# Optimization experiments

Hardware: AMD Instinct MI355X
Metric: run time of the kernel (lower is better)

Reference implementation:

```python
import jax, jax.numpy as jnp
import numpy as np

D_MODEL = 2048
NUM_HEADS = 16
D_KV = D_MODEL // NUM_HEADS
THETA = 10000.0


def apply_rope(x, pos):
    # x: [B, H, S, d_kv], pos: [S] int
    d = x.shape[-1]
    inv_freq = 1.0 / (THETA ** (jnp.arange(0, d, 2, dtype=jnp.float32) / d))  # [d/2]
    ang = pos.astype(jnp.float32)[:, None] * inv_freq[None, :]  # [S, d/2]
    cos, sin = jnp.cos(ang), jnp.sin(ang)  # broadcast over B,H
    x1 = x[..., 0::2]
    x2 = x[..., 1::2]
    r1 = x1 * cos - x2 * sin
    r2 = x1 * sin + x2 * cos
    return jnp.stack([r1, r2], axis=-1).reshape(x.shape)


def setup_inputs() -> dict:
    key = jax.random.key(0)
    k = jax.random.split(key, 5)
    B, S = 2, 2048
    x = jax.random.normal(k[0], (B, S, D_MODEL), dtype=jnp.float32)
    scale = 1.0 / np.sqrt(D_MODEL)
    Wq = jax.random.normal(k[1], (D_MODEL, D_MODEL), dtype=jnp.float32) * scale
    Wk = jax.random.normal(k[2], (D_MODEL, D_MODEL), dtype=jnp.float32) * scale
    Wv = jax.random.normal(k[3], (D_MODEL, D_MODEL), dtype=jnp.float32) * scale
    Wo = jax.random.normal(k[4], (D_MODEL, D_MODEL), dtype=jnp.float32) * scale
    token_position = jnp.arange(S, dtype=jnp.int64 if jax.config.jax_enable_x64 else jnp.int32)
    return {"x": x, "Wq": Wq, "Wk": Wk, "Wv": Wv, "Wo": Wo, "token_position": token_position}


def reference(x, Wq, Wk, Wv, Wo, token_position):
    B, S, _ = x.shape
    def heads(y):
        return y.reshape(B, S, NUM_HEADS, D_KV).transpose(0, 2, 1, 3)  # [B,H,S,d]
    Q = heads(jnp.einsum('bsd,df->bsf', x, Wq))
    K = heads(jnp.einsum('bsd,df->bsf', x, Wk))
    V = heads(jnp.einsum('bsd,df->bsf', x, Wv))
    Q = apply_rope(Q, token_position)
    K = apply_rope(K, token_position)
    scale = 1.0 / jnp.sqrt(jnp.asarray(D_KV, dtype=x.dtype))
    scores = jnp.einsum('bhqd,bhkd->bhqk', Q, K) * scale  # [B,H,S,S]
    causal = jnp.tril(jnp.ones((S, S), dtype=bool))
    scores = jnp.where(causal, scores, -jnp.inf)
    attn = jax.nn.softmax(scores, axis=-1)
    out = jnp.einsum('bhqk,bhkd->bhqd', attn, V)  # [B,H,S,d]
    out = out.transpose(0, 2, 1, 3).reshape(B, S, D_MODEL)
    return jnp.einsum('bsd,df->bsf', out, Wo)
```

## Files before the change

### kernel.cpp

```cpp
#include <hip/hip_runtime.h>

#define S 2048
#define DM 2048
#define NH 16
#define DH 128

typedef __attribute__((ext_vector_type(8))) short short8;
typedef __attribute__((ext_vector_type(4))) float floatx4;
typedef unsigned short u16;
typedef unsigned int u32;

__device__ __forceinline__ u16 f2bf(float f) {
  union { float f; u32 u; } v; v.f = f;
  u32 r = v.u + 0x7fffu + ((v.u >> 16) & 1u);
  return (u16)(r >> 16);
}
__device__ __forceinline__ u32 pack2(float lo, float hi) {
  return (u32)f2bf(lo) | ((u32)f2bf(hi) << 16);
}

__device__ __forceinline__ floatx4 mfma16(short8 a, short8 b, floatx4 c) {
  return __builtin_amdgcn_mfma_f32_16x16x32_bf16(a, b, c, 0, 0, 0);
}

__device__ __forceinline__ void async_cp16(const u16* g, u16* l) {
  __builtin_amdgcn_global_load_lds(
      (const __attribute__((address_space(1))) void*)g,
      (__attribute__((address_space(3))) void*)l, 16, 0, 0);
}

__global__ void conv_x_k(const float* __restrict__ x, u16* __restrict__ xb) {
  int gid = blockIdx.x * 256 + threadIdx.x;
  float4 v = ((const float4*)x)[gid];
  union { u16 u[4]; uint2 p; } o;
  o.u[0] = f2bf(v.x); o.u[1] = f2bf(v.y); o.u[2] = f2bf(v.z); o.u[3] = f2bf(v.w);
  ((uint2*)xb)[gid] = o.p;
}

__global__ void conv_w_k(const float* __restrict__ W0, const float* __restrict__ W1,
                         const float* __restrict__ W2, const float* __restrict__ W3,
                         u16* __restrict__ out) {
  __shared__ float tile[32][33];
  const float* W = blockIdx.z == 0 ? W0 : blockIdx.z == 1 ? W1 : blockIdx.z == 2 ? W2 : W3;
  u16* O = out + (size_t)blockIdx.z * DM * DM;
  int tx = threadIdx.x & 31, ty = threadIdx.x >> 5;
  int k0 = blockIdx.y * 32, n0 = blockIdx.x * 32;
#pragma unroll
  for (int j = 0; j < 4; j++)
    tile[ty + j * 8][tx] = W[(size_t)(k0 + ty + j * 8) * DM + n0 + tx];
  __syncthreads();
#pragma unroll
  for (int j = 0; j < 4; j++)
    O[(size_t)(n0 + ty + j * 8) * DM + k0 + tx] = f2bf(tile[tx][ty + j * 8]);
}

__global__ __launch_bounds__(256, 2)
void gemm_k(const u16* __restrict__ A, const u16* __restrict__ Wt,
            u16* __restrict__ oQ, u16* __restrict__ oK, u16* __restrict__ oV,
            float* __restrict__ oO, const int* __restrict__ tp, int opmode)
{
  __shared__ u16 As[128 * 32];
  __shared__ u16 Bs[128 * 32];
  const int t = threadIdx.x;
  const int w = t >> 6, lane = t & 63;
  const int l16 = lane & 15, quad = lane >> 4;
  const int m0 = blockIdx.y * 128, n0 = blockIdx.x * 128;
  const int wm = (w >> 1) * 64, wn = (w & 1) * 64;
  const u16* Bt = Wt + (size_t)(opmode == 1 ? 3 : blockIdx.z) * DM * DM;

  const u16* pA[2]; const u16* pB[2]; u16* lA[2]; u16* lB[2];
#pragma unroll
  for (int i = 0; i < 2; i++) {
    int unit = i * 256 + t;
    int row = unit >> 2, s = unit & 3;
    int c = s ^ ((row >> 1) & 3);
    pA[i] = A + (size_t)(m0 + row) * DM + c * 8;
    pB[i] = Bt + (size_t)(n0 + row) * DM + c * 8;
    lA[i] = &As[unit * 8];
    lB[i] = &Bs[unit * 8];
  }

  floatx4 acc[4][4] = {};

  for (int k0 = 0; k0 < DM; k0 += 32) {
#pragma unroll
    for (int i = 0; i < 2; i++) {
      async_cp16(pA[i] + k0, lA[i]);
      async_cp16(pB[i] + k0, lB[i]);
    }
    __syncthreads();
    short8 af[4], bfr[4];
#pragma unroll
    for (int i = 0; i < 4; i++) {
      int row = wm + i * 16 + l16;
      af[i] = *(short8*)&As[(row * 4 + (quad ^ ((row >> 1) & 3))) * 8];
    }
#pragma unroll
    for (int i = 0; i < 4; i++) {
      int row = wn + i * 16 + l16;
      bfr[i] = *(short8*)&Bs[(row * 4 + (quad ^ ((row >> 1) & 3))) * 8];
    }
#pragma unroll
    for (int mi = 0; mi < 4; mi++)
#pragma unroll
      for (int ni = 0; ni < 4; ni++)
        acc[mi][ni] = mfma16(af[mi], bfr[ni], acc[mi][ni]);
    __syncthreads();
  }

  const int mode = (opmode == 1) ? 3 : ((int)blockIdx.z == 2 ? 2 : 0);
  if (mode == 3) {
#pragma unroll
    for (int mi = 0; mi < 4; mi++) {
      int m = m0 + wm + mi * 16 + quad * 4;
#pragma unroll
      for (int ni = 0; ni < 4; ni++) {
        int n = n0 + wn + ni * 16 + l16;
#pragma unroll
        for (int r = 0; r < 4; r++)
          oO[(size_t)(m + r) * DM + n] = acc[mi][ni][r];
      }
    }
  } else if (mode == 2) {
#pragma unroll
    for (int mi = 0; mi < 4; mi++) {
      int m = m0 + wm + mi * 16 + quad * 4;
      int b = m >> 11, s = m & (S - 1);
#pragma unroll
      for (int ni = 0; ni < 4; ni++) {
        int f = n0 + wn + ni * 16 + l16;
        int h = f >> 7, dh = f & (DH - 1);
        union { u16 u[4]; uint2 p; } pk;
#pragma unroll
        for (int r = 0; r < 4; r++) pk.u[r] = f2bf(acc[mi][ni][r]);
        *(uint2*)&oV[((size_t)(b * NH + h) * DH + dh) * S + s] = pk.p;
      }
    }
  } else {
    u16* Out = ((int)blockIdx.z == 0) ? oQ : oK;
    const float qs = ((int)blockIdx.z == 0) ? 0.12752780f : 1.0f;
#pragma unroll
    for (int mi = 0; mi < 4; mi++) {
#pragma unroll
      for (int r = 0; r < 4; r++) {
        int m = m0 + wm + mi * 16 + quad * 4 + r;
        int b = m >> 11, s = m & (S - 1);
        int ps = tp[s];
#pragma unroll
        for (int ni = 0; ni < 4; ni++) {
          int f = n0 + wn + ni * 16 + l16;
          int h = f >> 7, dh = f & (DH - 1);
          float own = acc[mi][ni][r];
          float oth = __shfl_xor(own, 1, 64);
          float fr = __expf((float)(dh & ~1) * (-9.210340371976184f / 128.0f));
          float ang = (float)ps * fr;
          float sn, cs; __sincosf(ang, &sn, &cs);
          float res = (dh & 1) ? (oth * sn + own * cs) : (own * cs - oth * sn);
          Out[((size_t)(b * NH + h) * S + s) * DH + dh] = f2bf(res * qs);
        }
      }
    }
  }
}

__global__ __launch_bounds__(256, 3)
void attn_k(const u16* __restrict__ Q, const u16* __restrict__ K,
            const u16* __restrict__ Vt, u16* __restrict__ O)
{
  __shared__ u16 Ks[64 * 128];
  __shared__ u16 Vs[128 * 64];
  __shared__ u16 P[4][16 * 72];
  const int t = threadIdx.x, w = t >> 6, lane = t & 63;
  const int l16 = lane & 15, quad = lane >> 4;
  const int task = blockIdx.x;
  const int bh = task & 31, b = bh >> 4, h = bh & 15;
  const int g = 31 - (task >> 5);
  const int qg = g * 64;
  const int qt = qg + w * 16;
  const u16* Qb = Q + (size_t)bh * S * DH;
  const u16* Kb = K + (size_t)bh * S * DH;
  const u16* Vb = Vt + (size_t)bh * DH * S;
  u16* Pw = P[w];

  const u16* pK[4]; u16* lK[4];
  const u16* pV[4]; u16* lV[4];
#pragma unroll
  for (int j = 0; j < 4; j++) {
    int kr = w * 16 + j * 4 + (lane >> 4);
    int ks = lane & 15;
    int kc = ks ^ (kr & 15);
    pK[j] = Kb + (size_t)kr * DH + kc * 8;
    lK[j] = &Ks[kr * 128 + ks * 8];
    int vr = w * 32 + j * 8 + (lane >> 3);
    int vs = lane & 7;
    int vc = vs ^ (vr & 7);
    pV[j] = Vb + (size_t)vr * S + vc * 8;
    lV[j] = &Vs[vr * 64 + vs * 8];
  }

  short8 aq[4];
#pragma unroll
  for (int kc = 0; kc < 4; kc++)
    aq[kc] = *(const short8*)&Qb[(size_t)(qt + l16) * DH + kc * 32 + quad * 8];

  floatx4 o[8] = {};
  float m_ = -3.0e38f, l_ = 0.0f;
  const int kend = qg + 64;

  for (int k0 = 0; k0 < kend; k0 += 64) {
#pragma unroll
    for (int j = 0; j < 4; j++) async_cp16(pK[j] + (size_t)k0 * DH, lK[j]);
#pragma unroll
    for (int j = 0; j < 4; j++) async_cp16(pV[j] + k0, lV[j]);
    __syncthreads();

    floatx4 sc[4] = {};
#pragma unroll
    for (int hh = 0; hh < 4; hh++) {
      int row = hh * 16 + l16;
#pragma unroll
      for (int kc = 0; kc < 4; kc++) {
        short8 kf = *(short8*)&Ks[row * 128 + (((kc * 4 + quad) ^ l16) << 3)];
        sc[hh] = mfma16(kf, aq[kc], sc[hh]);
      }
    }
    if (k0 + 64 > qt) {
#pragma unroll
      for (int hh = 0; hh < 4; hh++)
#pragma unroll
        for (int r = 0; r < 4; r++) {
          int j = k0 + hh * 16 + quad * 4 + r;
          if (j > qt + l16) sc[hh][r] = -3.0e38f;
        }
    }
    float mloc = -3.0e38f;
#pragma unroll
    for (int hh = 0; hh < 4; hh++) {
      float a0 = fmaxf(sc[hh][0], sc[hh][1]);
      float a1 = fmaxf(sc[hh][2], sc[hh][3]);
      mloc = fmaxf(mloc, fmaxf(a0, a1));
    }
    mloc = fmaxf(mloc, __shfl_xor(mloc, 16, 64));
    mloc = fmaxf(mloc, __shfl_xor(mloc, 32, 64));
    float nm = fmaxf(m_, mloc);
    float al = __builtin_amdgcn_exp2f(m_ - nm);
    m_ = nm;
    float sloc = 0.0f;
    uint2 pk[4];
#pragma unroll
    for (int hh = 0; hh < 4; hh++) {
      float e0 = __builtin_amdgcn_exp2f(sc[hh][0] - nm);
      float e1 = __builtin_amdgcn_exp2f(sc[hh][1] - nm);
      float e2 = __builtin_amdgcn_exp2f(sc[hh][2] - nm);
      float e3 = __builtin_amdgcn_exp2f(sc[hh][3] - nm);
      sloc += (e0 + e1) + (e2 + e3);
      pk[hh].x = pack2(e0, e1);
      pk[hh].y = pack2(e2, e3);
    }
    float ts = sloc + __shfl_xor(sloc, 16, 64);
    ts += __shfl_xor(ts, 32, 64);
    l_ = l_ * al + ts;
#pragma unroll
    for (int t8 = 0; t8 < 8; t8++)
#pragma unroll
      for (int r = 0; r < 4; r++) o[t8][r] *= al;
#pragma unroll
    for (int hh = 0; hh < 4; hh++)
      *(uint2*)&Pw[l16 * 72 + hh * 16 + quad * 4] = pk[hh];
    asm volatile("s_waitcnt lgkmcnt(0)" ::: "memory");
#pragma unroll
    for (int c = 0; c < 2; c++) {
      short8 pf = *(short8*)&Pw[l16 * 72 + c * 32 + quad * 8];
#pragma unroll
      for (int t8 = 0; t8 < 8; t8++) {
        int row = t8 * 16 + l16;
        short8 av = *(short8*)&Vs[row * 64 + (((c * 4 + quad) ^ (l16 & 7)) << 3)];
        o[t8] = mfma16(av, pf, o[t8]);
      }
    }
    __syncthreads();
  }

  float inv = __builtin_amdgcn_rcpf(l_);
#pragma unroll
  for (int t8 = 0; t8 < 8; t8++) {
    union { u16 u[4]; uint2 p; } pk;
#pragma unroll
    for (int r = 0; r < 4; r++) pk.u[r] = f2bf(o[t8][r] * inv);
    *(uint2*)&O[((size_t)(b * S + qt + l16)) * DM + h * DH + t8 * 16 + quad * 4] = pk.p;
  }
}

extern "C" void kernel_launch(void* const* d_in, const int* in_sizes, int n_in,
                              void* d_out, int out_size, void* d_ws, size_t ws_size,
                              hipStream_t stream) {
  const float* x  = (const float*)d_in[0];
  const float* Wq = (const float*)d_in[1];
  const float* Wk = (const float*)d_in[2];
  const float* Wv = (const float*)d_in[3];
  const float* Wo = (const float*)d_in[4];
  const int*   tp = (const int*)d_in[5];

  char* ws = (char*)d_ws;
  u16* Wt = (u16*)ws;
  u16* xb = (u16*)(ws + 33554432);
  u16* Qb = (u16*)(ws + 50331648);
  u16* Kb = (u16*)(ws + 67108864);
  u16* Vb = (u16*)(ws + 83886080);
  u16* Ob = (u16*)(ws + 100663296);

  conv_x_k<<<8192, 256, 0, stream>>>(x, xb);
  conv_w_k<<<dim3(64, 64, 4), 256, 0, stream>>>(Wq, Wk, Wv, Wo, Wt);
  gemm_k<<<dim3(16, 32, 3), 256, 0, stream>>>(xb, Wt, Qb, Kb, Vb, nullptr, tp, 0);
  attn_k<<<1024, 256, 0, stream>>>(Qb, Kb, Vb, Ob);
  gemm_k<<<dim3(16, 32, 1), 256, 0, stream>>>(Ob, Wt, nullptr, nullptr, nullptr,
                                              (float*)d_out, tp, 1);
}
```

Baseline: 377.0 us.

## Process 32 query rows per warp in attention to reuse K/V tiles

The attention kernel now has each warp handle two 16-row query sub-tiles (128 queries per block), so every K and V fragment read from shared memory feeds two MFMAs. This halves the block count and K/V global traffic per query. Warps whose queries sit entirely before the current key tile skip compute. The trade-offs are doubled register state (two accumulator sets), a lower attn occupancy bound, and more causal-imbalance idle work inside a block. The GEMM launch bound is also raised to 4 waves per SIMD, which constrains register allocation.

```diff
diff --git a/kernel.cpp b/kernel.cpp
--- a/kernel.cpp
+++ b/kernel.cpp
@@ -54,7 +54,7 @@
     O[(size_t)(n0 + ty + j * 8) * DM + k0 + tx] = f2bf(tile[tx][ty + j * 8]);
 }
 
-__global__ __launch_bounds__(256, 2)
+__global__ __launch_bounds__(256, 4)
 void gemm_k(const u16* __restrict__ A, const u16* __restrict__ Wt,
             u16* __restrict__ oQ, u16* __restrict__ oK, u16* __restrict__ oV,
             float* __restrict__ oO, const int* __restrict__ tp, int opmode)
@@ -163,20 +163,20 @@
   }
 }
 
-__global__ __launch_bounds__(256, 3)
+__global__ __launch_bounds__(256, 2)
 void attn_k(const u16* __restrict__ Q, const u16* __restrict__ K,
             const u16* __restrict__ Vt, u16* __restrict__ O)
 {
   __shared__ u16 Ks[64 * 128];
   __shared__ u16 Vs[128 * 64];
-  __shared__ u16 P[4][16 * 72];
+  __shared__ u16 P[4][32 * 72];
   const int t = threadIdx.x, w = t >> 6, lane = t & 63;
   const int l16 = lane & 15, quad = lane >> 4;
   const int task = blockIdx.x;
   const int bh = task & 31, b = bh >> 4, h = bh & 15;
-  const int g = 31 - (task >> 5);
-  const int qg = g * 64;
-  const int qt = qg + w * 16;
+  const int g = 15 - (task >> 5);
+  const int qg = g * 128;
+  const int qt = qg + w * 32;
   const u16* Qb = Q + (size_t)bh * S * DH;
   const u16* Kb = K + (size_t)bh * S * DH;
   const u16* Vb = Vt + (size_t)bh * DH * S;
@@ -198,14 +198,16 @@
     lV[j] = &Vs[vr * 64 + vs * 8];
   }
 
-  short8 aq[4];
-#pragma unroll
-  for (int kc = 0; kc < 4; kc++)
-    aq[kc] = *(const short8*)&Qb[(size_t)(qt + l16) * DH + kc * 32 + quad * 8];
-
-  floatx4 o[8] = {};
-  float m_ = -3.0e38f, l_ = 0.0f;
-  const int kend = qg + 64;
+  short8 aq0[4], aq1[4];
+#pragma unroll
+  for (int kc = 0; kc < 4; kc++) {
+    aq0[kc] = *(const short8*)&Qb[(size_t)(qt + l16) * DH + kc * 32 + quad * 8];
+    aq1[kc] = *(const short8*)&Qb[(size_t)(qt + 16 + l16) * DH + kc * 32 + quad * 8];
+  }
+
+  floatx4 o0[8] = {}, o1[8] = {};
+  float m0_ = -3.0e38f, l0_ = 0.0f, m1_ = -3.0e38f, l1_ = 0.0f;
+  const int kend = qg + 128;
 
   for (int k0 = 0; k0 < kend; k0 += 64) {
 #pragma unroll
@@ -214,80 +216,115 @@
     for (int j = 0; j < 4; j++) async_cp16(pV[j] + k0, lV[j]);
     __syncthreads();
 
-    floatx4 sc[4] = {};
-#pragma unroll
-    for (int hh = 0; hh < 4; hh++) {
-      int row = hh * 16 + l16;
-#pragma unroll
-      for (int kc = 0; kc < 4; kc++) {
-        short8 kf = *(short8*)&Ks[row * 128 + (((kc * 4 + quad) ^ l16) << 3)];
-        sc[hh] = mfma16(kf, aq[kc], sc[hh]);
-      }
-    }
-    if (k0 + 64 > qt) {
-#pragma unroll
-      for (int hh = 0; hh < 4; hh++)
-#pragma unroll
-        for (int r = 0; r < 4; r++) {
-          int j = k0 + hh * 16 + quad * 4 + r;
-          if (j > qt + l16) sc[hh][r] = -3.0e38f;
-        }
-    }
-    float mloc = -3.0e38f;
-#pragma unroll
-    for (int hh = 0; hh < 4; hh++) {
-      float a0 = fmaxf(sc[hh][0], sc[hh][1]);
-      float a1 = fmaxf(sc[hh][2], sc[hh][3]);
-      mloc = fmaxf(mloc, fmaxf(a0, a1));
-    }
-    mloc = fmaxf(mloc, __shfl_xor(mloc, 16, 64));
-    mloc = fmaxf(mloc, __shfl_xor(mloc, 32, 64));
-    float nm = fmaxf(m_, mloc);
-    float al = __builtin_amdgcn_exp2f(m_ - nm);
-    m_ = nm;
-    float sloc = 0.0f;
-    uint2 pk[4];
-#pragma unroll
-    for (int hh = 0; hh < 4; hh++) {
-      float e0 = __builtin_amdgcn_exp2f(sc[hh][0] - nm);
-      float e1 = __builtin_amdgcn_exp2f(sc[hh][1] - nm);
-      float e2 = __builtin_amdgcn_exp2f(sc[hh][2] - nm);
-      float e3 = __builtin_amdgcn_exp2f(sc[hh][3] - nm);
-      sloc += (e0 + e1) + (e2 + e3);
-      pk[hh].x = pack2(e0, e1);
-      pk[hh].y = pack2(e2, e3);
-    }
-    float ts = sloc + __shfl_xor(sloc, 16, 64);
-    ts += __shfl_xor(ts, 32, 64);
-    l_ = l_ * al + ts;
-#pragma unroll
-    for (int t8 = 0; t8 < 8; t8++)
-#pragma unroll
-      for (int r = 0; r < 4; r++) o[t8][r] *= al;
-#pragma unroll
-    for (int hh = 0; hh < 4; hh++)
-      *(uint2*)&Pw[l16 * 72 + hh * 16 + quad * 4] = pk[hh];
-    asm volatile("s_waitcnt lgkmcnt(0)" ::: "memory");
-#pragma unroll
-    for (int c = 0; c < 2; c++) {
-      short8 pf = *(short8*)&Pw[l16 * 72 + c * 32 + quad * 8];
-#pragma unroll
-      for (int t8 = 0; t8 < 8; t8++) {
-        int row = t8 * 16 + l16;
-        short8 av = *(short8*)&Vs[row * 64 + (((c * 4 + quad) ^ (l16 & 7)) << 3)];
-        o[t8] = mfma16(av, pf, o[t8]);
+    if (k0 < qt + 32) {
+      floatx4 s0[4] = {}, s1[4] = {};
+#pragma unroll
+      for (int hh = 0; hh < 4; hh++) {
+        int row = hh * 16 + l16;
+#pragma unroll
+        for (int kc = 0; kc < 4; kc++) {
+          short8 kf = *(short8*)&Ks[row * 128 + (((kc * 4 + quad) ^ l16) << 3)];
+          s0[hh] = mfma16(kf, aq0[kc], s0[hh]);
+          s1[hh] = mfma16(kf, aq1[kc], s1[hh]);
+        }
+      }
+      if (k0 + 64 > qt) {
+#pragma unroll
+        for (int hh = 0; hh < 4; hh++)
+#pragma unroll
+          for (int r = 0; r < 4; r++) {
+            int j = k0 + hh * 16 + quad * 4 + r;
+            if (j > qt + l16) s0[hh][r] = -3.0e38f;
+            if (j > qt + 16 + l16) s1[hh][r] = -3.0e38f;
+          }
+      }
+      {
+        float mloc = -3.0e38f;
+#pragma unroll
+        for (int hh = 0; hh < 4; hh++)
+          mloc = fmaxf(mloc, fmaxf(fmaxf(s0[hh][0], s0[hh][1]), fmaxf(s0[hh][2], s0[hh][3])));
+        mloc = fmaxf(mloc, __shfl_xor(mloc, 16, 64));
+        mloc = fmaxf(mloc, __shfl_xor(mloc, 32, 64));
+        float nm = fmaxf(m0_, mloc);
+        float al = __builtin_amdgcn_exp2f(m0_ - nm);
+        m0_ = nm;
+        float sl = 0.0f;
+#pragma unroll
+        for (int hh = 0; hh < 4; hh++) {
+          float e0 = __builtin_amdgcn_exp2f(s0[hh][0] - nm);
+          float e1 = __builtin_amdgcn_exp2f(s0[hh][1] - nm);
+          float e2 = __builtin_amdgcn_exp2f(s0[hh][2] - nm);
+          float e3 = __builtin_amdgcn_exp2f(s0[hh][3] - nm);
+          sl += (e0 + e1) + (e2 + e3);
+          uint2 pk; pk.x = pack2(e0, e1); pk.y = pack2(e2, e3);
+          *(uint2*)&Pw[l16 * 72 + hh * 16 + quad * 4] = pk;
+        }
+        float ts = sl + __shfl_xor(sl, 16, 64);
+        ts += __shfl_xor(ts, 32, 64);
+        l0_ = l0_ * al + ts;
+#pragma unroll
+        for (int t8 = 0; t8 < 8; t8++)
+#pragma unroll
+          for (int r = 0; r < 4; r++) o0[t8][r] *= al;
+      }
+      {
+        float mloc = -3.0e38f;
+#pragma unroll
+        for (int hh = 0; hh < 4; hh++)
+          mloc = fmaxf(mloc, fmaxf(fmaxf(s1[hh][0], s1[hh][1]), fmaxf(s1[hh][2], s1[hh][3])));
+        mloc = fmaxf(mloc, __shfl_xor(mloc, 16, 64));
+        mloc = fmaxf(mloc, __shfl_xor(mloc, 32, 64));
+        float nm = fmaxf(m1_, mloc);
+        float al = __builtin_amdgcn_exp2f(m1_ - nm);
+        m1_ = nm;
+        float sl = 0.0f;
+#pragma unroll
+        for (int hh = 0; hh < 4; hh++) {
+          float e0 = __builtin_amdgcn_exp2f(s1[hh][0] - nm);
+          float e1 = __builtin_amdgcn_exp2f(s1[hh][1] - nm);
+          float e2 = __builtin_amdgcn_exp2f(s1[hh][2] - nm);
+          float e3 = __builtin_amdgcn_exp2f(s1[hh][3] - nm);
+          sl += (e0 + e1) + (e2 + e3);
+          uint2 pk; pk.x = pack2(e0, e1); pk.y = pack2(e2, e3);
+          *(uint2*)&Pw[(16 + l16) * 72 + hh * 16 + quad * 4] = pk;
+        }
+        float ts = sl + __shfl_xor(sl, 16, 64);
+        ts += __shfl_xor(ts, 32, 64);
+        l1_ = l1_ * al + ts;
+#pragma unroll
+        for (int t8 = 0; t8 < 8; t8++)
+#pragma unroll
+          for (int r = 0; r < 4; r++) o1[t8][r] *= al;
+      }
+      asm volatile("s_waitcnt lgkmcnt(0)" ::: "memory");
+#pragma unroll
+      for (int c = 0; c < 2; c++) {
+        short8 pf0 = *(short8*)&Pw[l16 * 72 + c * 32 + quad * 8];
+        short8 pf1 = *(short8*)&Pw[(16 + l16) * 72 + c * 32 + quad * 8];
+#pragma unroll
+        for (int t8 = 0; t8 < 8; t8++) {
+          int row = t8 * 16 + l16;
+          short8 av = *(short8*)&Vs[row * 64 + (((c * 4 + quad) ^ (l16 & 7)) << 3)];
+          o0[t8] = mfma16(av, pf0, o0[t8]);
+          o1[t8] = mfma16(av, pf1, o1[t8]);
+        }
       }
     }
     __syncthreads();
   }
 
-  float inv = __builtin_amdgcn_rcpf(l_);
+  float inv0 = __builtin_amdgcn_rcpf(l0_);
+  float inv1 = __builtin_amdgcn_rcpf(l1_);
 #pragma unroll
   for (int t8 = 0; t8 < 8; t8++) {
-    union { u16 u[4]; uint2 p; } pk;
-#pragma unroll
-    for (int r = 0; r < 4; r++) pk.u[r] = f2bf(o[t8][r] * inv);
-    *(uint2*)&O[((size_t)(b * S + qt + l16)) * DM + h * DH + t8 * 16 + quad * 4] = pk.p;
+    union { u16 u[4]; uint2 p; } pa, pb;
+#pragma unroll
+    for (int r = 0; r < 4; r++) {
+      pa.u[r] = f2bf(o0[t8][r] * inv0);
+      pb.u[r] = f2bf(o1[t8][r] * inv1);
+    }
+    *(uint2*)&O[((size_t)(b * S + qt + l16)) * DM + h * DH + t8 * 16 + quad * 4] = pa.p;
+    *(uint2*)&O[((size_t)(b * S + qt + 16 + l16)) * DM + h * DH + t8 * 16 + quad * 4] = pb.p;
   }
 }
 
@@ -312,7 +349,7 @@
   conv_x_k<<<8192, 256, 0, stream>>>(x, xb);
   conv_w_k<<<dim3(64, 64, 4), 256, 0, stream>>>(Wq, Wk, Wv, Wo, Wt);
   gemm_k<<<dim3(16, 32, 3), 256, 0, stream>>>(xb, Wt, Qb, Kb, Vb, nullptr, tp, 0);
-  attn_k<<<1024, 256, 0, stream>>>(Qb, Kb, Vb, Ob);
+  attn_k<<<512, 256, 0, stream>>>(Qb, Kb, Vb, Ob);
   gemm_k<<<dim3(16, 32, 1), 256, 0, stream>>>(Ob, Wt, nullptr, nullptr, nullptr,
                                               (float*)d_out, tp, 1);
 }
```

New measurement: 387.1 us. +2.7%, slower.
